# Kernel optimization log

Hardware: AMD Instinct MI355X
Metric: run time of the kernel (lower is better)

The kernel has to match this reference:

```python
import jax, jax.numpy as jnp
import numpy as np

Q_MAX = 127.0  # int8 symmetric range for activations


def setup_inputs() -> dict:
    key = jax.random.key(0)
    k1, k2, k3, k4 = jax.random.split(key, 4)
    B, S, D_IN, D_OUT = 4, 2048, 4096, 4096
    x = jax.random.normal(k1, (B, S, D_IN), dtype=jnp.float32)
    # int8 weights stored as int32 in range [-127, 127]
    w_q = jax.random.randint(k2, (D_OUT, D_IN), -127, 128, dtype=jnp.int32)
    # per-output-channel weight dequant scale (small positive)
    w_scale = jax.random.uniform(k3, (D_OUT,), dtype=jnp.float32, minval=0.001, maxval=0.02)
    b = jax.random.normal(k4, (D_OUT,), dtype=jnp.float32)
    return {"x": x, "w_q": w_q, "w_scale": w_scale, "b": b}


def reference(x, w_q, w_scale, b):
    # dynamic per-token symmetric quantization of activations
    act_scale = jnp.maximum(jnp.max(jnp.abs(x), axis=-1, keepdims=True), 1e-8) / Q_MAX  # [B,S,1]
    x_q = jnp.clip(jnp.round(x / act_scale), -128.0, 127.0)  # int8-valued float
    acc = jnp.einsum("bsk,nk->bsn", x_q, w_q.astype(jnp.float32))  # [B,S,D_OUT]
    # dequantize: per-token act scale * per-channel weight scale, then bias
    y = acc * act_scale * w_scale + b
    return y
```

## Files before the change

### kernel.cpp

```cpp
#include <hip/hip_runtime.h>
#include <hip/hip_bf16.h>
#include <stdint.h>

typedef int v4i __attribute__((ext_vector_type(4)));

#define TOK 8192
#define DIN 4096
#define DOUT 4096

#define NT 32

__global__ __launch_bounds__(256) void quant_rows(const float* __restrict__ x,
                                                  int8_t* __restrict__ xq,
                                                  float* __restrict__ ascale) {
    const int row = blockIdx.x;
    const int t = threadIdx.x;
    const float* __restrict__ xr = x + (size_t)row * DIN;
    float4 v[4];
    float amax = 0.0f;
#pragma unroll
    for (int i = 0; i < 4; ++i) {
        v[i] = reinterpret_cast<const float4*>(xr)[t + 256 * i];
        amax = fmaxf(amax, fmaxf(fmaxf(fabsf(v[i].x), fabsf(v[i].y)),
                                 fmaxf(fabsf(v[i].z), fabsf(v[i].w))));
    }
#pragma unroll
    for (int off = 1; off < 64; off <<= 1)
        amax = fmaxf(amax, __shfl_xor(amax, off, 64));
    __shared__ float wmax[4];
    if ((t & 63) == 0) wmax[t >> 6] = amax;
    __syncthreads();
    amax = fmaxf(fmaxf(wmax[0], wmax[1]), fmaxf(wmax[2], wmax[3]));
    const float scale = fmaxf(amax, 1e-8f) / 127.0f;
    if (t == 0) ascale[row] = scale;
    uint32_t* __restrict__ qr = reinterpret_cast<uint32_t*>(xq + (size_t)row * DIN);
#pragma unroll
    for (int i = 0; i < 4; ++i) {
        int q0 = (int)fminf(fmaxf(rintf(v[i].x / scale), -128.0f), 127.0f);
        int q1 = (int)fminf(fmaxf(rintf(v[i].y / scale), -128.0f), 127.0f);
        int q2 = (int)fminf(fmaxf(rintf(v[i].z / scale), -128.0f), 127.0f);
        int q3 = (int)fminf(fmaxf(rintf(v[i].w / scale), -128.0f), 127.0f);
        qr[t + 256 * i] = (uint32_t)((q0 & 0xFF) | ((q1 & 0xFF) << 8) |
                                     ((q2 & 0xFF) << 16) | ((q3 & 0xFF) << 24));
    }
}

__global__ __launch_bounds__(256) void pack_w(const int* __restrict__ wq,
                                              uint32_t* __restrict__ w8) {
    const size_t i = (size_t)blockIdx.x * 256 + threadIdx.x;
    int4 a = reinterpret_cast<const int4*>(wq)[i];
    w8[i] = (uint32_t)((a.x & 0xFF) | ((a.y & 0xFF) << 8) |
                       ((a.z & 0xFF) << 16) | ((a.w & 0xFF) << 24));
}

__global__ __launch_bounds__(512, 2) void gemm_i8(const int8_t* __restrict__ A,
                                                  const int8_t* __restrict__ B,
                                                  const float* __restrict__ ascale,
                                                  const float* __restrict__ wscale,
                                                  const float* __restrict__ bias,
                                                  float* __restrict__ C) {
    __shared__ __attribute__((aligned(16))) uint8_t lds[131072];
    const int tid = threadIdx.x;
    const int bn = blockIdx.x, bm = blockIdx.y;

    const int srow = tid >> 3;
    const int sp = tid & 7;
    const size_t soff0 = (size_t)srow * DIN + (size_t)(((sp ^ (srow & 7)) * 16));
    const size_t soff1 = soff0 + (size_t)64 * DIN;
    const uint32_t dst0 = (uint32_t)tid * 16u;
    const uint32_t dst1 = dst0 + 8192u;
    const int8_t* gA = A + (size_t)bm * 256 * DIN;
    const int8_t* gB = B + (size_t)bn * 256 * DIN;

#define STAGE_HALF(gmat, rbase, bufv, h, ktc)                                            \
    do {                                                                                 \
        const int8_t* _s = (gmat) + ((size_t)(h)*128 * DIN) + ((size_t)(ktc)*128);       \
        const uint32_t _d = (rbase) + (uint32_t)(bufv)*32768u + (uint32_t)(h)*16384u;    \
        __builtin_amdgcn_global_load_lds(                                                \
            (const __attribute__((address_space(1))) void*)(_s + soff0),                 \
            (__attribute__((address_space(3))) void*)(&lds[_d + dst0]), 16, 0, 0);       \
        __builtin_amdgcn_global_load_lds(                                                \
            (const __attribute__((address_space(1))) void*)(_s + soff1),                 \
            (__attribute__((address_space(3))) void*)(&lds[_d + dst1]), 16, 0, 0);       \
    } while (0)

    const int wid = tid >> 6, l = tid & 63;
    const int wm = (wid >> 2) * 128;
    const int wn = (wid & 3) * 64;
    const int lr = l & 15, lg = l >> 4;
    const uint32_t koff0 = (uint32_t)(((lg) ^ (l & 7)) * 16);
    const uint32_t koff1 = (uint32_t)(((4 + lg) ^ (l & 7)) * 16);
    const uint32_t aRd = (uint32_t)((wm >> 7) * 16384 + lr * 128);
    const uint32_t bRd = 65536u + (uint32_t)((wn >> 7) * 16384 + ((wn & 64) + lr) * 128);
    const uint32_t a0_0 = aRd + koff0, a1_0 = aRd + koff1;
    const uint32_t a0_1 = a0_0 + 32768u, a1_1 = a1_0 + 32768u;
    const uint32_t b0_0 = bRd + koff0, b1_0 = bRd + koff1;
    const uint32_t b0_1 = b0_0 + 32768u, b1_1 = b1_0 + 32768u;

    v4i acc[8][4];
#pragma unroll
    for (int i = 0; i < 8; ++i)
#pragma unroll
        for (int j = 0; j < 4; ++j) acc[i][j] = (v4i){0, 0, 0, 0};

    v4i aT[4][2], aB[4][2], bL[2][2], bR[2][2];

#define DSR(d, b, o) asm volatile("ds_read_b128 %0, %1 offset:" o : "=v"(d) : "v"(b))

#define RD_AT(A0, A1)                                          \
    do {                                                       \
        DSR(aT[0][0], A0, "0");     DSR(aT[0][1], A1, "0");    \
        DSR(aT[1][0], A0, "2048");  DSR(aT[1][1], A1, "2048"); \
        DSR(aT[2][0], A0, "4096");  DSR(aT[2][1], A1, "4096"); \
        DSR(aT[3][0], A0, "6144");  DSR(aT[3][1], A1, "6144"); \
    } while (0)
#define RD_AB(A0, A1)                                            \
    do {                                                         \
        DSR(aB[0][0], A0, "8192");  DSR(aB[0][1], A1, "8192");   \
        DSR(aB[1][0], A0, "10240"); DSR(aB[1][1], A1, "10240");  \
        DSR(aB[2][0], A0, "12288"); DSR(aB[2][1], A1, "12288");  \
        DSR(aB[3][0], A0, "14336"); DSR(aB[3][1], A1, "14336");  \
    } while (0)
#define RD_BL(B0, B1)                                          \
    do {                                                       \
        DSR(bL[0][0], B0, "0");    DSR(bL[0][1], B1, "0");     \
        DSR(bL[1][0], B0, "2048"); DSR(bL[1][1], B1, "2048");  \
    } while (0)
#define RD_BR(B0, B1)                                          \
    do {                                                       \
        DSR(bR[0][0], B0, "4096"); DSR(bR[0][1], B1, "4096");  \
        DSR(bR[1][0], B0, "6144"); DSR(bR[1][1], B1, "6144");  \
    } while (0)

#define BAR() asm volatile("s_barrier" ::: "memory")
#define LGKM0()                                                \
    do {                                                       \
        asm volatile("s_waitcnt lgkmcnt(0)" ::: "memory");     \
        __builtin_amdgcn_sched_barrier(0);                     \
    } while (0)
#define PRIO1() __builtin_amdgcn_s_setprio(1)
#define PRIO0()                                \
    do {                                       \
        __builtin_amdgcn_sched_barrier(0);     \
        __builtin_amdgcn_s_setprio(0);         \
    } while (0)
#define VM(n) asm volatile("s_waitcnt vmcnt(" #n ")" ::: "memory")

#define MFMA_K(AF, BF, MB, NB)                                                           \
    do {                                                                                 \
        _Pragma("unroll") for (int kk = 0; kk < 2; ++kk)                                 \
        _Pragma("unroll") for (int mi = 0; mi < 4; ++mi)                                 \
        _Pragma("unroll") for (int ni = 0; ni < 2; ++ni) {                               \
            acc[(MB) + mi][(NB) + ni] = __builtin_amdgcn_mfma_i32_16x16x64_i8(           \
                AF[mi][kk], BF[ni][kk], acc[(MB) + mi][(NB) + ni], 0, 0, 0);             \
        }                                                                                \
    } while (0)

    STAGE_HALF(gA, 0u, 0, 0, 0);
    STAGE_HALF(gA, 0u, 0, 1, 0);
    STAGE_HALF(gB, 65536u, 0, 0, 0);
    STAGE_HALF(gB, 65536u, 0, 1, 0);
    STAGE_HALF(gA, 0u, 1, 0, 1);
    STAGE_HALF(gA, 0u, 1, 1, 1);
    VM(4);

    for (int t = 0; t < NT / 2; ++t) {
        const int cv = 2 * t + 1;
        const int cu2 = (2 * t + 2 < NT) ? 2 * t + 2 : NT - 1;
        const int cv2 = (2 * t + 3 < NT) ? 2 * t + 3 : NT - 1;

        BAR();
        STAGE_HALF(gB, 65536u, 1, 0, cv);
        RD_AT(a0_0, a1_0); RD_BL(b0_0, b1_0);
        LGKM0();
        PRIO1();
        RD_AB(a0_0, a1_0); RD_BR(b0_0, b1_0);
        MFMA_K(aT, bL, 0, 0);
        PRIO0();

        BAR();
        STAGE_HALF(gB, 65536u, 1, 1, cv);
        LGKM0();
        PRIO1(); MFMA_K(aT, bR, 0, 2); PRIO0();

        BAR();
        STAGE_HALF(gA, 0u, 0, 0, cu2);
        LGKM0();
        PRIO1(); MFMA_K(aB, bL, 4, 0); PRIO0();

        BAR();
        STAGE_HALF(gA, 0u, 0, 1, cu2);
        LGKM0();
        PRIO1(); MFMA_K(aB, bR, 4, 2); PRIO0();
        VM(4);

        BAR();
        STAGE_HALF(gB, 65536u, 0, 0, cu2);
        RD_AT(a0_1, a1_1); RD_BL(b0_1, b1_1);
        LGKM0();
        PRIO1();
        RD_AB(a0_1, a1_1); RD_BR(b0_1, b1_1);
        MFMA_K(aT, bL, 0, 0);
        PRIO0();

        BAR();
        STAGE_HALF(gB, 65536u, 0, 1, cu2);
        LGKM0();
        PRIO1(); MFMA_K(aT, bR, 0, 2); PRIO0();

        BAR();
        STAGE_HALF(gA, 0u, 1, 0, cv2);
        LGKM0();
        PRIO1(); MFMA_K(aB, bL, 4, 0); PRIO0();

        BAR();
        STAGE_HALF(gA, 0u, 1, 1, cv2);
        LGKM0();
        PRIO1(); MFMA_K(aB, bR, 4, 2); PRIO0();
        VM(4);
    }

    asm volatile("s_waitcnt lgkmcnt(0)" ::: "memory");
    VM(0);

    const int col0 = bn * 256 + wn + lr;
    float wsv[4], bbv[4];
#pragma unroll
    for (int ni = 0; ni < 4; ++ni) {
        wsv[ni] = wscale[col0 + ni * 16];
        bbv[ni] = bias[col0 + ni * 16];
    }
    const int rbase = bm * 256 + wm + lg * 4;
#pragma unroll
    for (int mi = 0; mi < 8; ++mi) {
#pragma unroll
        for (int r = 0; r < 4; ++r) {
            const int row = rbase + mi * 16 + r;
            const float as = ascale[row];
            float* __restrict__ crow = C + (size_t)row * DOUT;
#pragma unroll
            for (int ni = 0; ni < 4; ++ni) {
                crow[col0 + ni * 16] = (float)acc[mi][ni][r] * as * wsv[ni] + bbv[ni];
            }
        }
    }
#undef STAGE_HALF
#undef DSR
#undef RD_AT
#undef RD_AB
#undef RD_BL
#undef RD_BR
#undef BAR
#undef LGKM0
#undef PRIO1
#undef PRIO0
#undef VM
#undef MFMA_K
}

extern "C" void kernel_launch(void* const* d_in, const int* in_sizes, int n_in,
                              void* d_out, int out_size, void* d_ws, size_t ws_size,
                              hipStream_t stream) {
    const float* x = (const float*)d_in[0];
    const int* wq = (const int*)d_in[1];
    const float* wscale = (const float*)d_in[2];
    const float* bias = (const float*)d_in[3];
    float* out = (float*)d_out;

    int8_t* xq = (int8_t*)d_ws;
    int8_t* w8 = xq + (size_t)TOK * DIN;
    float* ascale = (float*)(w8 + (size_t)DOUT * DIN);

    quant_rows<<<TOK, 256, 0, stream>>>(x, xq, ascale);
    pack_w<<<(int)(((size_t)DOUT * DIN / 4) / 256), 256, 0, stream>>>(wq, (uint32_t*)w8);
    gemm_i8<<<dim3(DOUT / 256, TOK / 256), 512, 0, stream>>>(xq, w8, ascale, wscale, bias, out);
}
```

Baseline: 183.0 us.

## Restructure int8 GEMM main loop into two phases with partial LDS waits

Collapses the eight barrier-separated sub-steps per double K-iteration into four phases (two per K tile), each staging a full pair of global-to-LDS halves. LDS reads are split by k-half and interleaved with MFMAs under graded lgkmcnt waits, so compute can begin before all fragments arrive. This halves the number of workgroup barriers and is meant to overlap ds_read latency with matrix math. The cost is larger bursts of global loads per phase and a more fragile hand-tuned ordering of waitcnt values, where a miscounted wait would consume stale registers.

```diff
diff --git a/kernel.cpp b/kernel.cpp
--- a/kernel.cpp
+++ b/kernel.cpp
@@ -107,36 +107,40 @@
 
 #define DSR(d, b, o) asm volatile("ds_read_b128 %0, %1 offset:" o : "=v"(d) : "v"(b))
 
-#define RD_AT(A0, A1)                                          \
+#define RD_AT0(A0)                                             \
     do {                                                       \
-        DSR(aT[0][0], A0, "0");     DSR(aT[0][1], A1, "0");    \
-        DSR(aT[1][0], A0, "2048");  DSR(aT[1][1], A1, "2048"); \
-        DSR(aT[2][0], A0, "4096");  DSR(aT[2][1], A1, "4096"); \
-        DSR(aT[3][0], A0, "6144");  DSR(aT[3][1], A1, "6144"); \
-    } while (0)
-#define RD_AB(A0, A1)                                            \
-    do {                                                         \
-        DSR(aB[0][0], A0, "8192");  DSR(aB[0][1], A1, "8192");   \
-        DSR(aB[1][0], A0, "10240"); DSR(aB[1][1], A1, "10240");  \
-        DSR(aB[2][0], A0, "12288"); DSR(aB[2][1], A1, "12288");  \
-        DSR(aB[3][0], A0, "14336"); DSR(aB[3][1], A1, "14336");  \
-    } while (0)
-#define RD_BL(B0, B1)                                          \
+        DSR(aT[0][0], A0, "0");    DSR(aT[1][0], A0, "2048");  \
+        DSR(aT[2][0], A0, "4096"); DSR(aT[3][0], A0, "6144");  \
+    } while (0)
+#define RD_AT1(A1)                                             \
     do {                                                       \
-        DSR(bL[0][0], B0, "0");    DSR(bL[0][1], B1, "0");     \
-        DSR(bL[1][0], B0, "2048"); DSR(bL[1][1], B1, "2048");  \
-    } while (0)
-#define RD_BR(B0, B1)                                          \
-    do {                                                       \
-        DSR(bR[0][0], B0, "4096"); DSR(bR[0][1], B1, "4096");  \
-        DSR(bR[1][0], B0, "6144"); DSR(bR[1][1], B1, "6144");  \
-    } while (0)
+        DSR(aT[0][1], A1, "0");    DSR(aT[1][1], A1, "2048");  \
+        DSR(aT[2][1], A1, "4096"); DSR(aT[3][1], A1, "6144");  \
+    } while (0)
+#define RD_AB0(A0)                                                \
+    do {                                                          \
+        DSR(aB[0][0], A0, "8192");  DSR(aB[1][0], A0, "10240");   \
+        DSR(aB[2][0], A0, "12288"); DSR(aB[3][0], A0, "14336");   \
+    } while (0)
+#define RD_AB1(A1)                                                \
+    do {                                                          \
+        DSR(aB[0][1], A1, "8192");  DSR(aB[1][1], A1, "10240");   \
+        DSR(aB[2][1], A1, "12288"); DSR(aB[3][1], A1, "14336");   \
+    } while (0)
+#define RD_BL0(B0)                                             \
+    do { DSR(bL[0][0], B0, "0"); DSR(bL[1][0], B0, "2048"); } while (0)
+#define RD_BL1(B1)                                             \
+    do { DSR(bL[0][1], B1, "0"); DSR(bL[1][1], B1, "2048"); } while (0)
+#define RD_BR0(B0)                                             \
+    do { DSR(bR[0][0], B0, "4096"); DSR(bR[1][0], B0, "6144"); } while (0)
+#define RD_BR1(B1)                                             \
+    do { DSR(bR[0][1], B1, "4096"); DSR(bR[1][1], B1, "6144"); } while (0)
 
 #define BAR() asm volatile("s_barrier" ::: "memory")
-#define LGKM0()                                                \
-    do {                                                       \
-        asm volatile("s_waitcnt lgkmcnt(0)" ::: "memory");     \
-        __builtin_amdgcn_sched_barrier(0);                     \
+#define LGKM(n)                                                     \
+    do {                                                            \
+        asm volatile("s_waitcnt lgkmcnt(" #n ")" ::: "memory");     \
+        __builtin_amdgcn_sched_barrier(0);                          \
     } while (0)
 #define PRIO1() __builtin_amdgcn_s_setprio(1)
 #define PRIO0()                                \
@@ -146,14 +150,48 @@
     } while (0)
 #define VM(n) asm volatile("s_waitcnt vmcnt(" #n ")" ::: "memory")
 
-#define MFMA_K(AF, BF, MB, NB)                                                           \
+#define MFMA_KK(AF, BF, MB, NB, KK)                                                      \
     do {                                                                                 \
-        _Pragma("unroll") for (int kk = 0; kk < 2; ++kk)                                 \
         _Pragma("unroll") for (int mi = 0; mi < 4; ++mi)                                 \
         _Pragma("unroll") for (int ni = 0; ni < 2; ++ni) {                               \
             acc[(MB) + mi][(NB) + ni] = __builtin_amdgcn_mfma_i32_16x16x64_i8(           \
-                AF[mi][kk], BF[ni][kk], acc[(MB) + mi][(NB) + ni], 0, 0, 0);             \
+                AF[mi][(KK)], BF[ni][(KK)], acc[(MB) + mi][(NB) + ni], 0, 0, 0);         \
         }                                                                                \
+    } while (0)
+
+#define PHASE_A(A0, A1, B0, B1, sbuf, ktc)          \
+    do {                                            \
+        BAR();                                      \
+        STAGE_HALF(gB, 65536u, sbuf, 0, ktc);       \
+        STAGE_HALF(gB, 65536u, sbuf, 1, ktc);       \
+        RD_AT0(A0); RD_BL0(B0);      \
+        RD_AT1(A1); RD_BL1(B1);      \
+        LGKM(6);                     \
+        PRIO1();                                    \
+        RD_BR0(B0); RD_BR1(B1);       \
+        RD_AB0(A0); RD_AB1(A1);       \
+        MFMA_KK(aT, bL, 0, 0, 0);        \
+        LGKM(12);                    \
+        MFMA_KK(aT, bL, 0, 0, 1);        \
+        LGKM(8);                     \
+        MFMA_KK(aT, bR, 0, 2, 0);        \
+        MFMA_KK(aT, bR, 0, 2, 1);        \
+        LGKM(0);                   \
+        PRIO0();                                    \
+    } while (0)
+
+#define PHASE_B(sbuf, ktc)                          \
+    do {                                            \
+        BAR();                                      \
+        STAGE_HALF(gA, 0u, sbuf, 0, ktc);           \
+        STAGE_HALF(gA, 0u, sbuf, 1, ktc);           \
+        PRIO1();                                    \
+        MFMA_KK(aB, bL, 4, 0, 0);                   \
+        MFMA_KK(aB, bL, 4, 0, 1);                   \
+        MFMA_KK(aB, bR, 4, 2, 0);                   \
+        MFMA_KK(aB, bR, 4, 2, 1);                   \
+        PRIO0();                                    \
+        VM(4);                                      \
     } while (0)
 
     STAGE_HALF(gA, 0u, 0, 0, 0);
@@ -169,58 +207,12 @@
         const int cu2 = (2 * t + 2 < NT) ? 2 * t + 2 : NT - 1;
         const int cv2 = (2 * t + 3 < NT) ? 2 * t + 3 : NT - 1;
 
-        BAR();
-        STAGE_HALF(gB, 65536u, 1, 0, cv);
-        RD_AT(a0_0, a1_0); RD_BL(b0_0, b1_0);
-        LGKM0();
-        PRIO1();
-        RD_AB(a0_0, a1_0); RD_BR(b0_0, b1_0);
-        MFMA_K(aT, bL, 0, 0);
-        PRIO0();
-
-        BAR();
-        STAGE_HALF(gB, 65536u, 1, 1, cv);
-        LGKM0();
-        PRIO1(); MFMA_K(aT, bR, 0, 2); PRIO0();
-
-        BAR();
-        STAGE_HALF(gA, 0u, 0, 0, cu2);
-        LGKM0();
-        PRIO1(); MFMA_K(aB, bL, 4, 0); PRIO0();
-
-        BAR();
-        STAGE_HALF(gA, 0u, 0, 1, cu2);
-        LGKM0();
-        PRIO1(); MFMA_K(aB, bR, 4, 2); PRIO0();
-        VM(4);
-
-        BAR();
-        STAGE_HALF(gB, 65536u, 0, 0, cu2);
-        RD_AT(a0_1, a1_1); RD_BL(b0_1, b1_1);
-        LGKM0();
-        PRIO1();
-        RD_AB(a0_1, a1_1); RD_BR(b0_1, b1_1);
-        MFMA_K(aT, bL, 0, 0);
-        PRIO0();
-
-        BAR();
-        STAGE_HALF(gB, 65536u, 0, 1, cu2);
-        LGKM0();
-        PRIO1(); MFMA_K(aT, bR, 0, 2); PRIO0();
-
-        BAR();
-        STAGE_HALF(gA, 0u, 1, 0, cv2);
-        LGKM0();
-        PRIO1(); MFMA_K(aB, bL, 4, 0); PRIO0();
-
-        BAR();
-        STAGE_HALF(gA, 0u, 1, 1, cv2);
-        LGKM0();
-        PRIO1(); MFMA_K(aB, bR, 4, 2); PRIO0();
-        VM(4);
-    }
-
-    asm volatile("s_waitcnt lgkmcnt(0)" ::: "memory");
+        PHASE_A(a0_0, a1_0, b0_0, b1_0, 1, cv);
+        PHASE_B(0, cu2);
+        PHASE_A(a0_1, a1_1, b0_1, b1_1, 0, cu2);
+        PHASE_B(1, cv2);
+    }
+
     VM(0);
 
     const int col0 = bn * 256 + wn + lr;
@@ -246,16 +238,22 @@
     }
 #undef STAGE_HALF
 #undef DSR
-#undef RD_AT
-#undef RD_AB
-#undef RD_BL
-#undef RD_BR
+#undef RD_AT0
+#undef RD_AT1
+#undef RD_AB0
+#undef RD_AB1
+#undef RD_BL0
+#undef RD_BL1
+#undef RD_BR0
+#undef RD_BR1
 #undef BAR
-#undef LGKM0
+#undef LGKM
 #undef PRIO1
 #undef PRIO0
 #undef VM
-#undef MFMA_K
+#undef MFMA_KK
+#undef PHASE_A
+#undef PHASE_B
 }
 
 extern "C" void kernel_launch(void* const* d_in, const int* in_sizes, int n_in,
```

New measurement: 182.3 us, median of 3. Within noise of the previous version (-0.4%).
